# Performance work log

Measured on AMD Instinct MI355X. Metric: run time of the kernel, lower is better.

## Reference

```python
import jax, jax.numpy as jnp
import numpy as np

M = 16384   # measurements (rows of A)
N = 65536   # signal dim (cols of A)
NNZ = 4194304
BATCH = 16
B_CLAMP = 1.0      # init kwarg B
NORM_EXP = 1.0     # init kwarg normalize=True -> exponent 1


def setup_inputs() -> dict:
    key = jax.random.key(0)
    k1, k2, k3, k4, k5, k6 = jax.random.split(key, 6)
    z = jax.random.normal(k1, (BATCH, N), dtype=jnp.float32)
    u = jax.random.normal(k2, (BATCH, N), dtype=jnp.float32)
    y = jax.random.normal(k3, (BATCH, M), dtype=jnp.float32)
    A_vals = jax.random.normal(k4, (NNZ,), dtype=jnp.float32)
    A_rows = jax.random.randint(k5, (NNZ,), 0, M, dtype=jnp.int32)
    A_cols = jax.random.randint(k6, (NNZ,), 0, N, dtype=jnp.int32)
    eta = jnp.full((1,), 0.001, dtype=jnp.float32)
    return {"z": z, "u": u, "y": y, "A_vals": A_vals,
            "A_rows": A_rows, "A_cols": A_cols, "eta": eta}


def _spmm_coo(x_T, gather_idx, scatter_idx, vals, num_segments):
    # x_T: [D_in, B]; out: [num_segments, B]. out[s,b] = sum_{k: scatter_idx[k]=s} vals[k]*x_T[gather_idx[k], b]
    contrib = vals[:, None] * jnp.take(x_T, gather_idx, axis=0)  # [nnz, B]
    return jax.ops.segment_sum(contrib, scatter_idx, num_segments=num_segments)


def reference(z, u, y, A_vals, A_rows, A_cols, eta):
    # t1 = (z*u) @ A^T : [B, M]
    zu = z * u
    t1 = _spmm_coo(zu.T, A_cols, A_rows, A_vals, M).T
    r = y - t1                                              # [B, M]
    # t2 = r @ A : [B, N]
    t2 = _spmm_coo(r.T, A_rows, A_cols, A_vals, N).T
    v = u * t2                                              # [B, N]
    # tf.norm over axis=1 of [B,N,1] == L2 norm over N
    v_norm = jnp.linalg.norm(v, axis=1, keepdims=True)      # [B, 1]
    v = v / jnp.maximum(1.0, v_norm / B_CLAMP) ** NORM_EXP
    return z - eta[0] * v
```

## Files before the change

### kernel.cpp

```cpp
#include <hip/hip_runtime.h>
#include <hip/hip_bf16.h>

#define MM   16384
#define NN   65536
#define NNZV 4194304
#define BB   16

#define NB    64
#define IPT   128
#define NBINS 8192
#define CAP   896


__global__ void k_zuT(const float* __restrict__ z, const float* __restrict__ u,
                      float* __restrict__ zuT) {
    int n = blockIdx.x * 256 + threadIdx.x;
    float f[BB];
#pragma unroll
    for (int b = 0; b < BB; ++b)
        f[b] = z[(size_t)b * NN + n] * u[(size_t)b * NN + n];
#pragma unroll
    for (int i = 0; i < 4; ++i)
        ((float4*)(zuT + (size_t)n * BB))[i] = ((float4*)f)[i];
}

__global__ __launch_bounds__(512) void k_hist(const int* __restrict__ sidx,
                                              const int* __restrict__ gidx,
                                              int* __restrict__ cnt,
                                              int ss, int gs, int ngt) {
    __shared__ int h[NBINS];
    for (int i = threadIdx.x; i < NBINS; i += 512) h[i] = 0;
    __syncthreads();
    int base = blockIdx.x * (512 * IPT);
    for (int it = 0; it < IPT; ++it) {
        int k = base + it * 512 + threadIdx.x;
        int bin = (sidx[k] >> ss) * ngt + (gidx[k] >> gs);
        atomicAdd(&h[bin], 1);
    }
    __syncthreads();
    for (int i = threadIdx.x; i < NBINS; i += 512)
        cnt[i * NB + blockIdx.x] = h[i];
}

__global__ __launch_bounds__(512) void k_scanA(int* __restrict__ cnt, int* __restrict__ bsum) {
    __shared__ int s[512];
    int tid = threadIdx.x;
    int v = cnt[blockIdx.x * 512 + tid];
    s[tid] = v;
    __syncthreads();
    for (int off = 1; off < 512; off <<= 1) {
        int t = (tid >= off) ? s[tid - off] : 0;
        __syncthreads();
        s[tid] += t;
        __syncthreads();
    }
    cnt[blockIdx.x * 512 + tid] = s[tid] - v;
    if (tid == 511) bsum[blockIdx.x] = s[511];
}

__global__ __launch_bounds__(1024) void k_scanB(int* __restrict__ bsum) {
    __shared__ int s[1024];
    int tid = threadIdx.x;
    int v = bsum[tid];
    s[tid] = v;
    __syncthreads();
    for (int off = 1; off < 1024; off <<= 1) {
        int t = (tid >= off) ? s[tid - off] : 0;
        __syncthreads();
        s[tid] += t;
        __syncthreads();
    }
    bsum[tid] = s[tid] - v;
}

__global__ __launch_bounds__(512) void k_scatter(const int* __restrict__ sidx,
                                                 const int* __restrict__ gidx,
                                                 const float* __restrict__ vals,
                                                 const int* __restrict__ cnt,
                                                 const int* __restrict__ bsum,
                                                 int ss, int gs, int ngt,
                                                 int smask, int gmask, int shl,
                                                 uint2* __restrict__ items) {
    __shared__ int nxt[NBINS];
    for (int i = threadIdx.x; i < NBINS; i += 512) {
        int idx = i * NB + blockIdx.x;
        nxt[i] = cnt[idx] + bsum[idx >> 9];
    }
    __syncthreads();
    int base = blockIdx.x * (512 * IPT);
    for (int it = 0; it < IPT; ++it) {
        int k = base + it * 512 + threadIdx.x;
        int s = sidx[k], g = gidx[k];
        float v = vals[k];
        int bin = (s >> ss) * ngt + (g >> gs);
        int r = atomicAdd(&nxt[bin], 1);
        items[r] = make_uint2(__float_as_uint(v),
                              ((unsigned)(g & gmask) << shl) | (unsigned)(s & smask));
    }
}

__global__ __launch_bounds__(512) void k_accumR(const uint2* __restrict__ items,
                                                const int* __restrict__ cnt,
                                                const int* __restrict__ bsum,
                                                const float* __restrict__ zuT,
                                                float* __restrict__ part) {
    __shared__ __align__(16) float stage[1024 * 16];
    __shared__ uint2 sortbuf[CAP];
    __shared__ int hist[128], starts[129], cursors[128], offs[33];
    int tid = threadIdx.x;
    int stile = blockIdx.x >> 1, split = blockIdx.x & 1;
    int fb = stile * 64 + split * 32;
    if (tid < 33) {
        int bin = fb + tid;
        offs[tid] = (bin < NBINS) ? (cnt[bin * NB] + bsum[(bin * NB) >> 9]) : NNZV;
    }
    int r_row = tid >> 2, q = tid & 3;
    float4 acc = make_float4(0.f, 0.f, 0.f, 0.f);
    float4 pf[8];
    {
        const float4* src = (const float4*)zuT + (size_t)(split * 32) * 4096;
#pragma unroll
        for (int r = 0; r < 8; ++r) pf[r] = src[r * 512 + tid];
    }
    __syncthreads();
#pragma unroll
    for (int r = 0; r < 8; ++r) ((float4*)stage)[r * 512 + tid] = pf[r];
    __syncthreads();
    for (int gi = 0; gi < 32; ++gi) {
        if (gi + 1 < 32) {
            const float4* src = (const float4*)zuT + (size_t)(split * 32 + gi + 1) * 4096;
#pragma unroll
            for (int r = 0; r < 8; ++r) pf[r] = src[r * 512 + tid];
        }
        int i0 = offs[gi], i1 = offs[gi + 1];
        if (tid < 128) hist[tid] = 0;
        __syncthreads();
        uint2 e0; bool have = (i0 + tid < i1);
        if (have) { e0 = items[i0 + tid]; atomicAdd(&hist[e0.y & 127u], 1); }
        for (int i = i0 + tid + 512; i < i1; i += 512)
            atomicAdd(&hist[items[i].y & 127u], 1);
        __syncthreads();
        if (tid < 64) {
            int b0 = tid * 2;
            int h0 = hist[b0], h1 = hist[b0 + 1];
            int s = h0 + h1, incl = s;
#pragma unroll
            for (int off = 1; off < 64; off <<= 1) {
                int v = __shfl_up(incl, off, 64);
                if (tid >= off) incl += v;
            }
            int excl = incl - s;
            starts[b0] = excl;      starts[b0 + 1] = excl + h0;
            cursors[b0] = excl;     cursors[b0 + 1] = excl + h0;
            if (tid == 63) starts[128] = incl;
        }
        __syncthreads();
        if (have) {
            int r = atomicAdd(&cursors[e0.y & 127u], 1);
            if (r < CAP) sortbuf[r] = e0;
        }
        for (int i = i0 + tid + 512; i < i1; i += 512) {
            uint2 e = items[i];
            int r = atomicAdd(&cursors[e.y & 127u], 1);
            if (r < CAP) sortbuf[r] = e;
        }
        __syncthreads();
        int js = starts[r_row], je = starts[r_row + 1];
        for (int j = js; j < je; ++j) {
            uint2 e = sortbuf[j];
            float v = __uint_as_float(e.x);
            int gl = (int)(e.y >> 7);
            float4 x = ((const float4*)stage)[gl * 4 + q];
            acc.x += v * x.x; acc.y += v * x.y; acc.z += v * x.z; acc.w += v * x.w;
        }
        __syncthreads();
        if (gi + 1 < 32) {
#pragma unroll
            for (int r = 0; r < 8; ++r) ((float4*)stage)[r * 512 + tid] = pf[r];
        }
        __syncthreads();
    }
    ((float4*)part)[((stile * 2 + split) * 128 + r_row) * 4 + q] = acc;
}

__global__ __launch_bounds__(512) void k_accumC(const uint2* __restrict__ items,
                                                const int* __restrict__ cnt,
                                                const int* __restrict__ bsum,
                                                const float* __restrict__ rT,
                                                float* __restrict__ t2T) {
    __shared__ __align__(16) float stage[512 * 16];
    __shared__ uint2 sortbuf[CAP];
    __shared__ int hist[256], starts[257], cursors[256], offs[33];
    int tid = threadIdx.x;
    int stile = blockIdx.x;
    int fb = stile * 32;
    if (tid < 33) {
        int bin = fb + tid;
        offs[tid] = (bin < NBINS) ? (cnt[bin * NB] + bsum[(bin * NB) >> 9]) : NNZV;
    }
    int r_row = tid >> 1, hh = tid & 1;
    float4 acc0 = make_float4(0.f, 0.f, 0.f, 0.f);
    float4 acc1 = make_float4(0.f, 0.f, 0.f, 0.f);
    float4 pf[4];
    {
        const float4* src = (const float4*)rT;
#pragma unroll
        for (int r = 0; r < 4; ++r) pf[r] = src[r * 512 + tid];
    }
    __syncthreads();
#pragma unroll
    for (int r = 0; r < 4; ++r) ((float4*)stage)[r * 512 + tid] = pf[r];
    __syncthreads();
    for (int gi = 0; gi < 32; ++gi) {
        if (gi + 1 < 32) {
            const float4* src = (const float4*)rT + (size_t)(gi + 1) * 2048;
#pragma unroll
            for (int r = 0; r < 4; ++r) pf[r] = src[r * 512 + tid];
        }
        int i0 = offs[gi], i1 = offs[gi + 1];
        if (tid < 256) hist[tid] = 0;
        __syncthreads();
        uint2 e0; bool have = (i0 + tid < i1);
        if (have) { e0 = items[i0 + tid]; atomicAdd(&hist[e0.y & 255u], 1); }
        for (int i = i0 + tid + 512; i < i1; i += 512)
            atomicAdd(&hist[items[i].y & 255u], 1);
        __syncthreads();
        if (tid < 64) {
            int b0 = tid * 4;
            int h0 = hist[b0], h1 = hist[b0 + 1], h2 = hist[b0 + 2], h3 = hist[b0 + 3];
            int s = h0 + h1 + h2 + h3, incl = s;
#pragma unroll
            for (int off = 1; off < 64; off <<= 1) {
                int v = __shfl_up(incl, off, 64);
                if (tid >= off) incl += v;
            }
            int excl = incl - s;
            starts[b0] = excl;          starts[b0 + 1] = excl + h0;
            starts[b0 + 2] = excl + h0 + h1; starts[b0 + 3] = excl + h0 + h1 + h2;
            cursors[b0] = starts[b0];   cursors[b0 + 1] = starts[b0 + 1];
            cursors[b0 + 2] = starts[b0 + 2]; cursors[b0 + 3] = starts[b0 + 3];
            if (tid == 63) starts[256] = incl;
        }
        __syncthreads();
        if (have) {
            int r = atomicAdd(&cursors[e0.y & 255u], 1);
            if (r < CAP) sortbuf[r] = e0;
        }
        for (int i = i0 + tid + 512; i < i1; i += 512) {
            uint2 e = items[i];
            int r = atomicAdd(&cursors[e.y & 255u], 1);
            if (r < CAP) sortbuf[r] = e;
        }
        __syncthreads();
        int js = starts[r_row], je = starts[r_row + 1];
        for (int j = js; j < je; ++j) {
            uint2 e = sortbuf[j];
            float v = __uint_as_float(e.x);
            int gl = (int)(e.y >> 8);
            float4 x0 = ((const float4*)stage)[gl * 4 + 2 * hh];
            float4 x1 = ((const float4*)stage)[gl * 4 + 2 * hh + 1];
            acc0.x += v * x0.x; acc0.y += v * x0.y; acc0.z += v * x0.z; acc0.w += v * x0.w;
            acc1.x += v * x1.x; acc1.y += v * x1.y; acc1.z += v * x1.z; acc1.w += v * x1.w;
        }
        __syncthreads();
        if (gi + 1 < 32) {
#pragma unroll
            for (int r = 0; r < 4; ++r) ((float4*)stage)[r * 512 + tid] = pf[r];
        }
        __syncthreads();
    }
    ((float4*)t2T)[(stile * 256 + r_row) * 4 + 2 * hh]     = acc0;
    ((float4*)t2T)[(stile * 256 + r_row) * 4 + 2 * hh + 1] = acc1;
}

__global__ __launch_bounds__(256) void k_reduce_rT(const float* __restrict__ y,
                                                   const float* __restrict__ part,
                                                   float* __restrict__ rT) {
    int id = blockIdx.x * 256 + threadIdx.x;
    int m = id >> 2, q = id & 3;
    int stile = m >> 7, l = m & 127;
    const float4* p4 = (const float4*)part;
    float4 s0 = p4[((stile * 2 + 0) * 128 + l) * 4 + q];
    float4 s1 = p4[((stile * 2 + 1) * 128 + l) * 4 + q];
    float4 o;
    o.x = y[(size_t)(4 * q + 0) * MM + m] - (s0.x + s1.x);
    o.y = y[(size_t)(4 * q + 1) * MM + m] - (s0.y + s1.y);
    o.z = y[(size_t)(4 * q + 2) * MM + m] - (s0.z + s1.z);
    o.w = y[(size_t)(4 * q + 3) * MM + m] - (s0.w + s1.w);
    ((float4*)rT)[m * 4 + q] = o;
}

__global__ __launch_bounds__(256) void k_norm(const float* __restrict__ u,
                                              const float* __restrict__ t2T,
                                              float* __restrict__ partials) {
    __shared__ float wsum[4][BB];
    int n = blockIdx.x * 256 + threadIdx.x;
    float t[BB];
#pragma unroll
    for (int i = 0; i < 4; ++i)
        ((float4*)t)[i] = ((const float4*)(t2T + (size_t)n * BB))[i];
    float acc[BB];
#pragma unroll
    for (int b = 0; b < BB; ++b) {
        float v = u[(size_t)b * NN + n] * t[b];
        acc[b] = v * v;
    }
#pragma unroll
    for (int b = 0; b < BB; ++b) {
#pragma unroll
        for (int off = 32; off; off >>= 1)
            acc[b] += __shfl_xor(acc[b], off, 64);
    }
    int wid = threadIdx.x >> 6, lane = threadIdx.x & 63;
    if (lane < BB) wsum[wid][lane] = acc[lane];
    __syncthreads();
    if (threadIdx.x < BB) {
        float s = wsum[0][threadIdx.x] + wsum[1][threadIdx.x]
                + wsum[2][threadIdx.x] + wsum[3][threadIdx.x];
        partials[blockIdx.x * BB + threadIdx.x] = s;
    }
}

__global__ __launch_bounds__(256) void k_normfin(const float* __restrict__ partials,
                                                 float* __restrict__ norm2) {
    __shared__ float s[256];
    int tid = threadIdx.x;
    int b = tid & 15, grp = tid >> 4;
    float a = 0.f;
    for (int i = grp; i < 256; i += 16) a += partials[i * BB + b];
    s[tid] = a;
    __syncthreads();
    if (tid < BB) {
        float t = 0.f;
#pragma unroll
        for (int g = 0; g < 16; ++g) t += s[g * 16 + tid];
        norm2[tid] = t;
    }
}

__global__ void k_final(const float* __restrict__ z, const float* __restrict__ u,
                        const float* __restrict__ t2T, const float* __restrict__ norm2,
                        const float* __restrict__ eta, float* __restrict__ out) {
    int n = blockIdx.x * 256 + threadIdx.x;
    float t[BB];
#pragma unroll
    for (int i = 0; i < 4; ++i)
        ((float4*)t)[i] = ((const float4*)(t2T + (size_t)n * BB))[i];
    float e = eta[0];
#pragma unroll
    for (int b = 0; b < BB; ++b) {
        float denom = fmaxf(1.0f, sqrtf(norm2[b]));
        float v = u[(size_t)b * NN + n] * t[b];
        out[(size_t)b * NN + n] = z[(size_t)b * NN + n] - e * v / denom;
    }
}

extern "C" void kernel_launch(void* const* d_in, const int* in_sizes, int n_in,
                              void* d_out, int out_size, void* d_ws, size_t ws_size,
                              hipStream_t stream) {
    const float* z      = (const float*)d_in[0];
    const float* u      = (const float*)d_in[1];
    const float* y      = (const float*)d_in[2];
    const float* A_vals = (const float*)d_in[3];
    const int*   A_rows = (const int*)d_in[4];
    const int*   A_cols = (const int*)d_in[5];
    const float* eta    = (const float*)d_in[6];
    float* out = (float*)d_out;

    char* ws = (char*)d_ws;
    float* norm2 = (float*)(ws);
    float* nparts = (float*)(ws + 256);
    int*   bsum  = (int*)  (ws + 65536);
    float* r0    = (float*)(ws + (1u << 20));
    float* rT    = (float*)(ws + (5u << 20));
    float* part  = (float*)(ws + (6u << 20));
    int*   cnt   = (int*)  (ws + (8u << 20));
    uint2* items = (uint2*)(ws + (10u << 20));

    k_zuT<<<NN / 256, 256, 0, stream>>>(z, u, r0);
    k_hist<<<NB, 512, 0, stream>>>(A_rows, A_cols, cnt, 7, 10, 64);
    k_scanA<<<1024, 512, 0, stream>>>(cnt, bsum);
    k_scanB<<<1, 1024, 0, stream>>>(bsum);
    k_scatter<<<NB, 512, 0, stream>>>(A_rows, A_cols, A_vals, cnt, bsum,
                                      7, 10, 64, 127, 1023, 7, items);
    k_accumR<<<256, 512, 0, stream>>>(items, cnt, bsum, r0, part);
    k_reduce_rT<<<256, 256, 0, stream>>>(y, part, rT);

    k_hist<<<NB, 512, 0, stream>>>(A_cols, A_rows, cnt, 8, 9, 32);
    k_scanA<<<1024, 512, 0, stream>>>(cnt, bsum);
    k_scanB<<<1, 1024, 0, stream>>>(bsum);
    k_scatter<<<NB, 512, 0, stream>>>(A_cols, A_rows, A_vals, cnt, bsum,
                                      8, 9, 32, 255, 511, 8, items);
    k_accumC<<<256, 512, 0, stream>>>(items, cnt, bsum, rT, r0);

    k_norm<<<NN / 256, 256, 0, stream>>>(u, r0, nparts);
    k_normfin<<<1, 256, 0, stream>>>(nparts, norm2);
    k_final<<<NN / 256, 256, 0, stream>>>(z, u, r0, norm2, eta, out);
}
```

Baseline: 840.3 us.

## Replace per-row counting sort with per-wave segment bucketing and masked accumulation

Result: slower. 978.9 us (+16.5%).

```diff
diff --git a/kernel.cpp b/kernel.cpp
--- a/kernel.cpp
+++ b/kernel.cpp
@@ -9,7 +9,7 @@
 #define NB    64
 #define IPT   128
 #define NBINS 8192
-#define CAP   896
+#define CAP2  192
 
 
 __global__ void k_zuT(const float* __restrict__ z, const float* __restrict__ u,
@@ -105,16 +105,18 @@
                                                 const float* __restrict__ zuT,
                                                 float* __restrict__ part) {
     __shared__ __align__(16) float stage[1024 * 16];
-    __shared__ uint2 sortbuf[CAP];
-    __shared__ int hist[128], starts[129], cursors[128], offs[33];
-    int tid = threadIdx.x;
+    __shared__ uint2 seg[8][CAP2];
+    __shared__ int cur[8];
+    __shared__ int offs[33];
+    int tid = threadIdx.x, wid = tid >> 6, lane = tid & 63;
     int stile = blockIdx.x >> 1, split = blockIdx.x & 1;
     int fb = stile * 64 + split * 32;
     if (tid < 33) {
         int bin = fb + tid;
         offs[tid] = (bin < NBINS) ? (cnt[bin * NB] + bsum[(bin * NB) >> 9]) : NNZV;
     }
-    int r_row = tid >> 2, q = tid & 3;
+    if (tid < 8) cur[tid] = 0;
+    int r_lane = lane >> 2, q = lane & 3;
     float4 acc = make_float4(0.f, 0.f, 0.f, 0.f);
     float4 pf[8];
     {
@@ -133,54 +135,31 @@
             for (int r = 0; r < 8; ++r) pf[r] = src[r * 512 + tid];
         }
         int i0 = offs[gi], i1 = offs[gi + 1];
-        if (tid < 128) hist[tid] = 0;
-        __syncthreads();
-        uint2 e0; bool have = (i0 + tid < i1);
-        if (have) { e0 = items[i0 + tid]; atomicAdd(&hist[e0.y & 127u], 1); }
-        for (int i = i0 + tid + 512; i < i1; i += 512)
-            atomicAdd(&hist[items[i].y & 127u], 1);
-        __syncthreads();
-        if (tid < 64) {
-            int b0 = tid * 2;
-            int h0 = hist[b0], h1 = hist[b0 + 1];
-            int s = h0 + h1, incl = s;
-#pragma unroll
-            for (int off = 1; off < 64; off <<= 1) {
-                int v = __shfl_up(incl, off, 64);
-                if (tid >= off) incl += v;
-            }
-            int excl = incl - s;
-            starts[b0] = excl;      starts[b0 + 1] = excl + h0;
-            cursors[b0] = excl;     cursors[b0 + 1] = excl + h0;
-            if (tid == 63) starts[128] = incl;
-        }
-        __syncthreads();
-        if (have) {
-            int r = atomicAdd(&cursors[e0.y & 127u], 1);
-            if (r < CAP) sortbuf[r] = e0;
-        }
-        for (int i = i0 + tid + 512; i < i1; i += 512) {
+        for (int i = i0 + tid; i < i1; i += 512) {
             uint2 e = items[i];
-            int r = atomicAdd(&cursors[e.y & 127u], 1);
-            if (r < CAP) sortbuf[r] = e;
-        }
-        __syncthreads();
-        int js = starts[r_row], je = starts[r_row + 1];
-        for (int j = js; j < je; ++j) {
-            uint2 e = sortbuf[j];
+            int rg = (int)((e.y >> 4) & 7u);
+            int p = atomicAdd(&cur[rg], 1);
+            if (p < CAP2) seg[rg][p] = e;
+        }
+        __syncthreads();
+        int cw = cur[wid]; if (cw > CAP2) cw = CAP2;
+        for (int j = 0; j < cw; ++j) {
+            uint2 e = seg[wid][j];
             float v = __uint_as_float(e.x);
+            float vm = ((int)(e.y & 15u) == r_lane) ? v : 0.f;
             int gl = (int)(e.y >> 7);
             float4 x = ((const float4*)stage)[gl * 4 + q];
-            acc.x += v * x.x; acc.y += v * x.y; acc.z += v * x.z; acc.w += v * x.w;
-        }
-        __syncthreads();
+            acc.x += vm * x.x; acc.y += vm * x.y; acc.z += vm * x.z; acc.w += vm * x.w;
+        }
+        __syncthreads();
+        if (tid < 8) cur[tid] = 0;
         if (gi + 1 < 32) {
 #pragma unroll
             for (int r = 0; r < 8; ++r) ((float4*)stage)[r * 512 + tid] = pf[r];
         }
         __syncthreads();
     }
-    ((float4*)part)[((stile * 2 + split) * 128 + r_row) * 4 + q] = acc;
+    ((float4*)part)[((stile * 2 + split) * 128 + wid * 16 + r_lane) * 4 + q] = acc;
 }
 
 __global__ __launch_bounds__(512) void k_accumC(const uint2* __restrict__ items,
@@ -189,18 +168,19 @@
                                                 const float* __restrict__ rT,
                                                 float* __restrict__ t2T) {
     __shared__ __align__(16) float stage[512 * 16];
-    __shared__ uint2 sortbuf[CAP];
-    __shared__ int hist[256], starts[257], cursors[256], offs[33];
-    int tid = threadIdx.x;
-    int stile = blockIdx.x;
+    __shared__ uint2 seg[8][CAP2];
+    __shared__ int cur[8];
+    __shared__ int offs[33];
+    int tid = threadIdx.x, wid = tid >> 6, lane = tid & 63;
+    int stile = blockIdx.x >> 1, bh = blockIdx.x & 1;
     int fb = stile * 32;
     if (tid < 33) {
         int bin = fb + tid;
         offs[tid] = (bin < NBINS) ? (cnt[bin * NB] + bsum[(bin * NB) >> 9]) : NNZV;
     }
-    int r_row = tid >> 1, hh = tid & 1;
-    float4 acc0 = make_float4(0.f, 0.f, 0.f, 0.f);
-    float4 acc1 = make_float4(0.f, 0.f, 0.f, 0.f);
+    if (tid < 8) cur[tid] = 0;
+    int c_lane = lane >> 1, h = lane & 1, qsel = 2 * bh + h;
+    float4 acc = make_float4(0.f, 0.f, 0.f, 0.f);
     float4 pf[4];
     {
         const float4* src = (const float4*)rT;
@@ -218,59 +198,32 @@
             for (int r = 0; r < 4; ++r) pf[r] = src[r * 512 + tid];
         }
         int i0 = offs[gi], i1 = offs[gi + 1];
-        if (tid < 256) hist[tid] = 0;
-        __syncthreads();
-        uint2 e0; bool have = (i0 + tid < i1);
-        if (have) { e0 = items[i0 + tid]; atomicAdd(&hist[e0.y & 255u], 1); }
-        for (int i = i0 + tid + 512; i < i1; i += 512)
-            atomicAdd(&hist[items[i].y & 255u], 1);
-        __syncthreads();
-        if (tid < 64) {
-            int b0 = tid * 4;
-            int h0 = hist[b0], h1 = hist[b0 + 1], h2 = hist[b0 + 2], h3 = hist[b0 + 3];
-            int s = h0 + h1 + h2 + h3, incl = s;
-#pragma unroll
-            for (int off = 1; off < 64; off <<= 1) {
-                int v = __shfl_up(incl, off, 64);
-                if (tid >= off) incl += v;
-            }
-            int excl = incl - s;
-            starts[b0] = excl;          starts[b0 + 1] = excl + h0;
-            starts[b0 + 2] = excl + h0 + h1; starts[b0 + 3] = excl + h0 + h1 + h2;
-            cursors[b0] = starts[b0];   cursors[b0 + 1] = starts[b0 + 1];
-            cursors[b0 + 2] = starts[b0 + 2]; cursors[b0 + 3] = starts[b0 + 3];
-            if (tid == 63) starts[256] = incl;
-        }
-        __syncthreads();
-        if (have) {
-            int r = atomicAdd(&cursors[e0.y & 255u], 1);
-            if (r < CAP) sortbuf[r] = e0;
-        }
-        for (int i = i0 + tid + 512; i < i1; i += 512) {
+        for (int i = i0 + tid; i < i1; i += 512) {
             uint2 e = items[i];
-            int r = atomicAdd(&cursors[e.y & 255u], 1);
-            if (r < CAP) sortbuf[r] = e;
-        }
-        __syncthreads();
-        int js = starts[r_row], je = starts[r_row + 1];
-        for (int j = js; j < je; ++j) {
-            uint2 e = sortbuf[j];
+            int rg = (int)((e.y >> 5) & 7u);
+            int p = atomicAdd(&cur[rg], 1);
+            if (p < CAP2) seg[rg][p] = e;
+        }
+        __syncthreads();
+        int cw = cur[wid]; if (cw > CAP2) cw = CAP2;
+        for (int j = 0; j < cw; ++j) {
+            uint2 e = seg[wid][j];
             float v = __uint_as_float(e.x);
+            float vm = ((int)(e.y & 31u) == c_lane) ? v : 0.f;
             int gl = (int)(e.y >> 8);
-            float4 x0 = ((const float4*)stage)[gl * 4 + 2 * hh];
-            float4 x1 = ((const float4*)stage)[gl * 4 + 2 * hh + 1];
-            acc0.x += v * x0.x; acc0.y += v * x0.y; acc0.z += v * x0.z; acc0.w += v * x0.w;
-            acc1.x += v * x1.x; acc1.y += v * x1.y; acc1.z += v * x1.z; acc1.w += v * x1.w;
-        }
-        __syncthreads();
+            float4 x = ((const float4*)stage)[gl * 4 + qsel];
+            acc.x += vm * x.x; acc.y += vm * x.y; acc.z += vm * x.z; acc.w += vm * x.w;
+        }
+        __syncthreads();
+        if (tid < 8) cur[tid] = 0;
         if (gi + 1 < 32) {
 #pragma unroll
             for (int r = 0; r < 4; ++r) ((float4*)stage)[r * 512 + tid] = pf[r];
         }
         __syncthreads();
     }
-    ((float4*)t2T)[(stile * 256 + r_row) * 4 + 2 * hh]     = acc0;
-    ((float4*)t2T)[(stile * 256 + r_row) * 4 + 2 * hh + 1] = acc1;
+    int col = stile * 256 + wid * 32 + c_lane;
+    ((float4*)t2T)[col * 4 + qsel] = acc;
 }
 
 __global__ __launch_bounds__(256) void k_reduce_rT(const float* __restrict__ y,
@@ -391,7 +344,7 @@
     k_scanB<<<1, 1024, 0, stream>>>(bsum);
     k_scatter<<<NB, 512, 0, stream>>>(A_cols, A_rows, A_vals, cnt, bsum,
                                       8, 9, 32, 255, 511, 8, items);
-    k_accumC<<<256, 512, 0, stream>>>(items, cnt, bsum, rT, r0);
+    k_accumC<<<512, 512, 0, stream>>>(items, cnt, bsum, rT, r0);
 
     k_norm<<<NN / 256, 256, 0, stream>>>(u, r0, nparts);
     k_normfin<<<1, 256, 0, stream>>>(nparts, norm2);
```
